# Performance work log

Hardware: AMD Instinct MI355X
Metric: run time of the kernel (lower is better)

The kernel has to match this reference:

```python
import math
import jax, jax.numpy as jnp
import numpy as np

B, N, D_MODEL, H = 2, 4096, 2048, 16
HEAD_DIM = D_MODEL // H
CHUNK = 128  # chunk length for the lightning-attention recurrence


def _slopes(n_heads):
    # ALiBi-style slopes used by lightning attention (n_heads is a power of 2)
    start = 2.0 ** (-(2.0 ** -(math.log2(n_heads) - 3)))
    return np.array([start ** (i + 1) for i in range(n_heads)], dtype=np.float32)


def setup_inputs() -> dict:
    key = jax.random.key(0)
    kx, k1, k2, k3, k4 = jax.random.split(key, 5)
    scale = 1.0 / math.sqrt(D_MODEL)
    x = jax.random.normal(kx, (B, N, D_MODEL), dtype=jnp.float32)
    w_qkv = jax.random.normal(k1, (3 * D_MODEL, D_MODEL), dtype=jnp.float32) * scale
    b_qkv = jax.random.normal(k2, (3 * D_MODEL,), dtype=jnp.float32) * 0.01
    w_out = jax.random.normal(k3, (D_MODEL, D_MODEL), dtype=jnp.float32) * scale
    b_out = jax.random.normal(k4, (D_MODEL,), dtype=jnp.float32) * 0.01
    return {"x": x, "w_qkv": w_qkv, "b_qkv": b_qkv, "w_out": w_out, "b_out": b_out}


def _lightning_attn(q, k, v):
    # q,k,v: (B, H, N, d). Causal linear attention with per-head decay lam:
    #   S_t = lam * S_{t-1} + k_t v_t^T ;  o_t = q_t S_t
    b, h, n, d = q.shape
    nc = n // CHUNK
    lam = jnp.exp(-jnp.asarray(_slopes(h)))  # (H,)

    pos = jnp.arange(CHUNK, dtype=jnp.float32)
    decay_q = lam[:, None] ** (pos + 1.0)            # (H, C) inter-chunk q scaling
    decay_k = lam[:, None] ** (CHUNK - 1.0 - pos)    # (H, C) state-update k scaling
    diff = pos[:, None] - pos[None, :]
    causal = diff >= 0
    dmask = jnp.where(causal, lam[:, None, None] ** jnp.maximum(diff, 0.0), 0.0)  # (H,C,C)
    lam_c = lam ** CHUNK                              # (H,)

    def to_chunks(t):
        return t.reshape(b, h, nc, CHUNK, d).transpose(2, 0, 1, 3, 4)  # (nc,B,H,C,d)

    qc, kc, vc = to_chunks(q), to_chunks(k), to_chunks(v)

    def step(S, inp):
        qb, kb, vb = inp  # each (B,H,C,d); S: (B,H,d,d)
        inter = jnp.einsum('bhcd,bhde->bhce', qb * decay_q[None, :, :, None], S)
        scores = jnp.einsum('bhcd,bhed->bhce', qb, kb) * dmask[None]
        intra = jnp.einsum('bhce,bhed->bhcd', scores, vb)
        S_new = lam_c[None, :, None, None] * S + jnp.einsum(
            'bhcd,bhce->bhde', kb * decay_k[None, :, :, None], vb)
        return S_new, inter + intra

    S0 = jnp.zeros((b, h, d, d), dtype=q.dtype)
    _, out = jax.lax.scan(step, S0, (qc, kc, vc))  # out: (nc,B,H,C,d)
    return out.transpose(1, 2, 0, 3, 4).reshape(b, h, n, d)


def reference(x, w_qkv, b_qkv, w_out, b_out):
    b, n, dm = x.shape
    qkv = x @ w_qkv.T + b_qkv                         # (B,N,3D)
    q, k, v = jnp.split(qkv, 3, axis=-1)
    def heads(t):
        return t.reshape(b, n, H, HEAD_DIM).transpose(0, 2, 1, 3)  # (B,H,N,d)
    attn = _lightning_attn(heads(q), heads(k), heads(v))
    attn = attn.transpose(0, 2, 1, 3).reshape(b, n, dm)
    return attn @ w_out.T + b_out
```

## Files before the change

### kernel.cpp

```cpp
#include <hip/hip_runtime.h>
#include <stdint.h>

#define DM    2048
#define NSEQ  4096
#define BB    2
#define NH    16
#define HD    128
#define CHK   128
#define NCHK  32
#define NBH   (BB*NH)
#define MTOT  (BB*NSEQ)
#define N3    (3*DM)

typedef unsigned short u16;
typedef unsigned int   u32;
typedef __attribute__((ext_vector_type(8))) short s16x8;
typedef __attribute__((ext_vector_type(4))) short s16x4;
typedef __attribute__((ext_vector_type(4))) float f32x4;
typedef __attribute__((ext_vector_type(2))) unsigned short u16x2;

__device__ __forceinline__ float b2f(u16 b){ u32 u = ((u32)b) << 16; float f; __builtin_memcpy(&f,&u,4); return f; }
__device__ __forceinline__ u16 f2b(float f){ u32 u; __builtin_memcpy(&u,&f,4); u += 0x7fffu + ((u>>16)&1u); return (u16)(u>>16); }

__device__ __forceinline__ void gload16(const u16* g, u16* l){
  __builtin_amdgcn_global_load_lds((const __attribute__((address_space(1))) void*)g,
                                   (__attribute__((address_space(3))) void*)l, 16, 0, 0);
}

__global__ __launch_bounds__(256) void conv_bf16(const float* __restrict__ src,
                                                 u16* __restrict__ dst, int n4)
{
  for (int i = blockIdx.x*blockDim.x + threadIdx.x; i < n4; i += gridDim.x*blockDim.x){
    f32x4 v = *(const f32x4*)(src + (size_t)i*4);
    s16x4 o;
    #pragma unroll
    for (int j=0;j<4;j++) o[j] = (short)f2b(v[j]);
    *(s16x4*)(dst + (size_t)i*4) = o;
  }
}


#define GEMM256_CORE(GA_, GB_)                                                  \
  const int tid  = threadIdx.x;                                                 \
  const int lane = tid & 63;                                                    \
  const int w    = tid >> 6;                                                    \
  const int wm_i = w >> 2, wn_i = w & 3;                                        \
  int bx = blockIdx.x, by = blockIdx.y;                                         \
  { const int gx = gridDim.x; const int nwg = gx*gridDim.y;                     \
    const int cpx = nwg >> 3; const int lin = by*gx + bx;                       \
    const int t_ = (lin & 7)*cpx + (lin >> 3);                                  \
    bx = t_ % gx; by = t_ / gx; }                                               \
  const int m0 = by << 8;                                                       \
  const int n0 = bx << 8;                                                       \
                  \
  const int q_  = (lane*16) ^ (((lane>>5)&1) << 5);                             \
  const int sgr = q_ >> 6;                                                      \
  const int sgc = (q_ & 63) >> 1;                                               \
  const u16* gA = GA_ + (size_t)(m0 + w*32 + sgr)*DM + sgc;                     \
  const u16* gB = GB_ + (size_t)(n0 + w*32 + sgr)*DM + sgc;                     \
  const int l15 = lane & 15, lg = lane >> 4;                                    \
  const int swz = ((lg*16) ^ (((l15>>3)&1) << 5)) >> 1;          \
  const int arow = (wm_i*128 + l15)*32 + swz;                                   \
  const int brow = (wn_i*64  + l15)*32 + swz;                                   \
  f32x4 acc[8][4];                                                              \
  _Pragma("unroll")                                                             \
  for (int m=0;m<8;m++)                                                         \
    _Pragma("unroll")                                                           \
    for (int n=0;n<4;n++) acc[m][n] = f32x4{0.f,0.f,0.f,0.f};                   \
  auto STAGE_A = [&](int set, int kt){                                          \
    const u16* a = gA + kt*32;                                                  \
    u16* la = lds + set + w*1024;                                               \
    gload16(a,         la);                                                     \
    gload16(a + 16*DM, la + 512);                                               \
  };                                                                            \
  auto STAGE_B = [&](int set, int kt){                                          \
    const u16* b = gB + kt*32;                                                  \
    u16* la = lds + set + w*1024;                                               \
    gload16(b,         la + 8192);                                              \
    gload16(b + 16*DM, la + 8704);                                              \
  };                                                                            \
  STAGE_A(0, 0);     STAGE_B(0, 0);                                             \
  STAGE_A(16384, 1); STAGE_B(16384, 1);                                         \
  STAGE_A(32768, 2); STAGE_B(32768, 2);                                         \
  asm volatile("s_waitcnt vmcnt(8)" ::: "memory");                              \
  __builtin_amdgcn_s_barrier();                                                 \
  int s0=0, s1=16384, s2=32768, s3=49152;                                       \
  for (int t=0; t<64; ++t){                                                     \
    const u16* base = lds + s0;                                                 \
         \
    s16x8 af0[4], af1[4], bfr[4];                                               \
    _Pragma("unroll")                                                           \
    for (int n=0;n<4;n++) bfr[n] = *(const s16x8*)(base + 8192 + brow + n*512); \
    _Pragma("unroll")                                                           \
    for (int m=0;m<4;m++) af0[m] = *(const s16x8*)(base + arow + m*512);        \
    if (t < 61) STAGE_A(s3, t+3);                                               \
    __builtin_amdgcn_sched_barrier(0);                                          \
    __builtin_amdgcn_s_barrier();                                               \
    asm volatile("s_waitcnt lgkmcnt(0)" ::: "memory");                          \
    __builtin_amdgcn_sched_barrier(0);                                          \
    __builtin_amdgcn_s_setprio(1);                                              \
    _Pragma("unroll")                                                           \
    for (int m=0;m<4;m++)                                                       \
      _Pragma("unroll")                                                         \
      for (int n=0;n<4;n++)                                                     \
        acc[m][n] = __builtin_amdgcn_mfma_f32_16x16x32_bf16(af0[m], bfr[n], acc[m][n], 0,0,0); \
    __builtin_amdgcn_s_setprio(0);                                              \
    __builtin_amdgcn_sched_barrier(0);                                          \
    __builtin_amdgcn_s_barrier();                                               \
      \
    _Pragma("unroll")                                                           \
    for (int m=0;m<4;m++) af1[m] = *(const s16x8*)(base + arow + (m+4)*512);    \
    if (t < 61) STAGE_B(s3, t+3);                                               \
    if      (t < 61)  { asm volatile("s_waitcnt vmcnt(8)" ::: "memory"); }      \
    else if (t == 61) { asm volatile("s_waitcnt vmcnt(4)" ::: "memory"); }      \
    else if (t == 62) { asm volatile("s_waitcnt vmcnt(0)" ::: "memory"); }      \
    __builtin_amdgcn_sched_barrier(0);                                          \
    __builtin_amdgcn_s_barrier();                                               \
    asm volatile("s_waitcnt lgkmcnt(0)" ::: "memory");                          \
    __builtin_amdgcn_sched_barrier(0);                                          \
    __builtin_amdgcn_s_setprio(1);                                              \
    _Pragma("unroll")                                                           \
    for (int m=0;m<4;m++)                                                       \
      _Pragma("unroll")                                                         \
      for (int n=0;n<4;n++)                                                     \
        acc[m+4][n] = __builtin_amdgcn_mfma_f32_16x16x32_bf16(af1[m], bfr[n], acc[m+4][n], 0,0,0); \
    __builtin_amdgcn_s_setprio(0);                                              \
    __builtin_amdgcn_sched_barrier(0);                                          \
    __builtin_amdgcn_s_barrier();                                               \
    const int tmp=s0; s0=s1; s1=s2; s2=s3; s3=tmp;                              \
  }

__global__ __launch_bounds__(512, 2) void gemm_qkv(const u16* __restrict__ Xb,
    const u16* __restrict__ Wb, const float* __restrict__ bias,
    u16* __restrict__ Qb, u16* __restrict__ Kb, u16* __restrict__ Vb)
{
  __shared__ u16 lds[4*16384];
  GEMM256_CORE(Xb, Wb)

  #pragma unroll
  for (int n=0;n<4;n++){
    const int gn = n0 + wn_i*64 + n*16 + l15;
    const float bv = bias[gn];
    const int which = gn >> 11;
    const int h = (gn >> 7) & 15;
    const int e = gn & 127;
    u16* base_ = (which==0) ? Qb : ((which==1) ? Kb : Vb);
    #pragma unroll
    for (int m=0;m<8;m++){
      #pragma unroll
      for (int r=0;r<4;r++){
        const int gm = m0 + wm_i*128 + m*16 + lg*4 + r;
        const int b  = gm >> 12;
        const int tt = gm & (NSEQ-1);
        base_[(((size_t)(b*NH + h))*NSEQ + tt)*HD + e] = f2b(acc[m][n][r] + bv);
      }
    }
  }
}

__global__ __launch_bounds__(512, 2) void gemm_out(const u16* __restrict__ Ab,
    const u16* __restrict__ Wb, const float* __restrict__ bias,
    float* __restrict__ Out)
{
  __shared__ u16 lds[4*16384];
  GEMM256_CORE(Ab, Wb)

  #pragma unroll
  for (int n=0;n<4;n++){
    const int gn = n0 + wn_i*64 + n*16 + l15;
    const float bv = bias[gn];
    #pragma unroll
    for (int m=0;m<8;m++){
      #pragma unroll
      for (int r=0;r<4;r++){
        const int gm = m0 + wm_i*128 + m*16 + lg*4 + r;
        Out[(size_t)gm*DM + gn] = acc[m][n][r] + bv;
      }
    }
  }
}

__global__ __launch_bounds__(256) void chunk_kv(const u16* __restrict__ Kb,
    const u16* __restrict__ Vb, u16* __restrict__ USb)
{
  __shared__ short Kt[128][152];
  __shared__ short Vt[128][152];
  const int tid = threadIdx.x;
  const int blk = blockIdx.x;
  const int c  = blk & (NCHK-1);
  const int bh = blk >> 5;
  const int h  = bh & (NH-1);
  const float slope = exp2f(-0.5f*(float)(h+1));

  const u16* kg = Kb + ((size_t)bh*NSEQ + (size_t)c*CHK)*HD;
  const u16* vg = Vb + ((size_t)bh*NSEQ + (size_t)c*CHK)*HD;

  const int e0 = (tid & 63) * 2;
  const int tq = tid >> 6;
  #pragma unroll
  for (int it=0; it<4; it++){
    const int tb = it*32 + tq*8;
    s16x8 k0v, k1v, v0v, v1v;
    #pragma unroll
    for (int j=0;j<8;j++){
      const int t = tb + j;
      u16x2 kv = *(const u16x2*)(kg + (size_t)t*HD + e0);
      u16x2 vv = *(const u16x2*)(vg + (size_t)t*HD + e0);
      const float dk = expf(-slope*(float)(CHK-1-t));
      k0v[j] = (short)f2b(b2f(kv[0])*dk);
      k1v[j] = (short)f2b(b2f(kv[1])*dk);
      v0v[j] = (short)vv[0];
      v1v[j] = (short)vv[1];
    }
    *(s16x8*)&Kt[e0  ][tb] = k0v;
    *(s16x8*)&Kt[e0+1][tb] = k1v;
    *(s16x8*)&Vt[e0  ][tb] = v0v;
    *(s16x8*)&Vt[e0+1][tb] = v1v;
  }
  __syncthreads();

  const int lane = tid & 63;
  const int l15 = lane & 15, lg = lane >> 4;
  const int w = tid >> 6;
  const int wm = (w >> 1) << 6, wn = (w & 1) << 6;
  f32x4 acc[4][4];
  #pragma unroll
  for (int i=0;i<4;i++)
    #pragma unroll
    for (int j=0;j<4;j++) acc[i][j] = f32x4{0.f,0.f,0.f,0.f};

  #pragma unroll
  for (int ks=0; ks<4; ks++){
    const int kk = ks*32 + lg*8;
    s16x8 af[4], bf[4];
    #pragma unroll
    for (int m=0;m<4;m++) af[m] = *(const s16x8*)&Kt[wm + m*16 + l15][kk];
    #pragma unroll
    for (int n=0;n<4;n++) bf[n] = *(const s16x8*)&Vt[wn + n*16 + l15][kk];
    #pragma unroll
    for (int m=0;m<4;m++)
      #pragma unroll
      for (int n=0;n<4;n++)
        acc[m][n] = __builtin_amdgcn_mfma_f32_16x16x32_bf16(af[m], bf[n], acc[m][n], 0,0,0);
  }

  u16* up = USb + (size_t)blk*(HD*HD);
  #pragma unroll
  for (int m=0;m<4;m++)
    #pragma unroll
    for (int n=0;n<4;n++)
      #pragma unroll
      for (int r=0;r<4;r++){
        const int d = wm + m*16 + lg*4 + r;
        const int f = wn + n*16 + l15;
        up[d*HD + f] = f2b(acc[m][n][r]);
      }
}

__global__ __launch_bounds__(256) void scan_state(u16* __restrict__ USb)
{
  const int bh = blockIdx.x >> 3;
  const int rs = blockIdx.x & 7;
  const int tid = threadIdx.x;
  const int h = bh & (NH-1);
  const float slope = exp2f(-0.5f*(float)(h+1));
  const float lamC = expf(-slope*(float)CHK);
  float s[8];
  #pragma unroll
  for (int i=0;i<8;i++) s[i]=0.f;
  u16* base = USb + (size_t)bh*NCHK*HD*HD + rs*2048;
  const int off = tid*8;
  for (int c=0;c<NCHK;c++){
    u16* p = base + (size_t)c*HD*HD + off;
    s16x8 u = *(const s16x8*)p;
    s16x8 wv;
    #pragma unroll
    for (int j=0;j<8;j++) wv[j] = (short)f2b(s[j]);
    *(s16x8*)p = wv;
    #pragma unroll
    for (int j=0;j<8;j++) s[j] = lamC*s[j] + b2f((u16)u[j]);
  }
}

__global__ __launch_bounds__(512) void attn_chunk(
    const u16* __restrict__ Qb, const u16* __restrict__ Kb, const u16* __restrict__ Vb,
    const u16* __restrict__ Sb, u16* __restrict__ ATT)
{
  __shared__ short lds[73728];
  short* Qs = lds;
  short* Ks = lds + 17408;
  short* Vt = lds + 34816;
  short* St = lds + 54272;

  const int tid = threadIdx.x;
  const int blk = blockIdx.x;
  const int c  = blk & (NCHK-1);
  const int bh = blk >> 5;
  const int b  = bh >> 4, h = bh & 15;
  const float slope = exp2f(-0.5f*(float)(h+1));

  const size_t qoff = ((size_t)bh*NSEQ + (size_t)c*CHK)*HD;

  #pragma unroll
  for (int i=0;i<4;i++){
    const int lin = i*4096 + tid*8;
    const int r = lin >> 7, e = lin & 127;
    *(s16x8*)&Qs[r*136 + e] = *(const s16x8*)(Qb + qoff + lin);
    *(s16x8*)&Ks[r*136 + e] = *(const s16x8*)(Kb + qoff + lin);
  }
  {
    const int f0 = (tid & 63)*2;
    const int tq = tid >> 6;
    const u16* vg = Vb + qoff;
    const u16* sg = Sb + ((size_t)bh*NCHK + c)*HD*HD;
    #pragma unroll
    for (int it=0; it<2; it++){
      const int t0 = it*64 + tq*8;
      s16x8 v0v, v1v, s0v, s1v;
      #pragma unroll
      for (int j=0;j<8;j++){
        u16x2 v2 = *(const u16x2*)(vg + (size_t)(t0+j)*HD + f0);
        u16x2 s2 = *(const u16x2*)(sg + (size_t)(t0+j)*HD + f0);
        v0v[j]=(short)v2[0]; v1v[j]=(short)v2[1];
        s0v[j]=(short)s2[0]; s1v[j]=(short)s2[1];
      }
      *(s16x8*)&Vt[(f0  )*152 + t0] = v0v;
      *(s16x8*)&Vt[(f0+1)*152 + t0] = v1v;
      *(s16x8*)&St[(f0  )*152 + t0] = s0v;
      *(s16x8*)&St[(f0+1)*152 + t0] = s1v;
    }
  }
  __syncthreads();

  const int lane = tid & 63;
  const int l15 = lane & 15, lg = lane >> 4;
  const int w = tid >> 6;
  const int wrow = (w >> 1) << 5;
  const int wcol = (w & 1) << 6;

  f32x4 accs[2][4], acco[2][4];
  #pragma unroll
  for (int m=0;m<2;m++)
    #pragma unroll
    for (int n=0;n<4;n++){ accs[m][n]=f32x4{0.f,0.f,0.f,0.f}; acco[m][n]=f32x4{0.f,0.f,0.f,0.f}; }

  #pragma unroll
  for (int ks=0; ks<4; ks++){
    const int kk = ks*32 + lg*8;
    s16x8 qa[2], kb_[4], sb_[4];
    #pragma unroll
    for (int m=0;m<2;m++) qa[m] = *(const s16x8*)&Qs[(wrow + m*16 + l15)*136 + kk];
    #pragma unroll
    for (int n=0;n<4;n++){
      kb_[n] = *(const s16x8*)&Ks[(wcol + n*16 + l15)*136 + kk];
      sb_[n] = *(const s16x8*)&St[(wcol + n*16 + l15)*152 + kk];
    }
    #pragma unroll
    for (int m=0;m<2;m++)
      #pragma unroll
      for (int n=0;n<4;n++){
        accs[m][n] = __builtin_amdgcn_mfma_f32_16x16x32_bf16(qa[m], kb_[n], accs[m][n], 0,0,0);
        acco[m][n] = __builtin_amdgcn_mfma_f32_16x16x32_bf16(qa[m], sb_[n], acco[m][n], 0,0,0);
      }
  }
  __syncthreads();

  #pragma unroll
  for (int m=0;m<2;m++){
    #pragma unroll
    for (int r=0;r<4;r++){
      const int t = wrow + m*16 + lg*4 + r;
      const float dq = expf(-slope*(float)(t+1));
      #pragma unroll
      for (int n=0;n<4;n++){
        const int s = wcol + n*16 + l15;
        float v = accs[m][n][r];
        v = (t >= s) ? v*expf(-slope*(float)(t-s)) : 0.f;
        Ks[t*136 + s] = (short)f2b(v);
        acco[m][n][r] *= dq;
      }
    }
  }
  __syncthreads();

  #pragma unroll
  for (int ks=0; ks<4; ks++){
    const int kk = ks*32 + lg*8;
    s16x8 sa[2], vb_[4];
    #pragma unroll
    for (int m=0;m<2;m++) sa[m] = *(const s16x8*)&Ks[(wrow + m*16 + l15)*136 + kk];
    #pragma unroll
    for (int n=0;n<4;n++) vb_[n] = *(const s16x8*)&Vt[(wcol + n*16 + l15)*152 + kk];
    #pragma unroll
    for (int m=0;m<2;m++)
      #pragma unroll
      for (int n=0;n<4;n++)
        acco[m][n] = __builtin_amdgcn_mfma_f32_16x16x32_bf16(sa[m], vb_[n], acco[m][n], 0,0,0);
  }

  u16* op = ATT + ((size_t)(b*NSEQ + c*CHK))*DM + h*HD;
  #pragma unroll
  for (int m=0;m<2;m++)
    #pragma unroll
    for (int n=0;n<4;n++)
      #pragma unroll
      for (int r=0;r<4;r++){
        const int t = wrow + m*16 + lg*4 + r;
        const int f = wcol + n*16 + l15;
        op[(size_t)t*DM + f] = f2b(acco[m][n][r]);
      }
}

extern "C" void kernel_launch(void* const* d_in, const int* in_sizes, int n_in,
                              void* d_out, int out_size, void* d_ws, size_t ws_size,
                              hipStream_t stream)
{
  const float* x     = (const float*)d_in[0];
  const float* w_qkv = (const float*)d_in[1];
  const float* b_qkv = (const float*)d_in[2];
  const float* w_out = (const float*)d_in[3];
  const float* b_out = (const float*)d_in[4];
  float* out = (float*)d_out;

  char* ws = (char*)d_ws;
  const size_t SZ = (size_t)MTOT * DM * sizeof(u16);
  u16* Qb    = (u16*)(ws);
  u16* Kb    = (u16*)(ws + SZ);
  u16* Vb    = (u16*)(ws + 2*SZ);
  u16* USb   = (u16*)(ws + 3*SZ);
  u16* ATT   = (u16*)(ws + 4*SZ);
  u16* Xb    = ATT;
  u16* Wqkvb = USb;
  u16* Woutb = Kb;

  conv_bf16 <<<dim3(2048), 256, 0, stream>>>(x,     Xb,    MTOT*DM/4);
  conv_bf16 <<<dim3(2048), 256, 0, stream>>>(w_qkv, Wqkvb, N3*DM/4);
  gemm_qkv  <<<dim3(N3/256,  MTOT/256), 512, 0, stream>>>(Xb, Wqkvb, b_qkv, Qb, Kb, Vb);
  chunk_kv  <<<dim3(NBH*NCHK),          256, 0, stream>>>(Kb, Vb, USb);
  scan_state<<<dim3(NBH*8),             256, 0, stream>>>(USb);
  attn_chunk<<<dim3(NBH*NCHK),          512, 0, stream>>>(Qb, Kb, Vb, USb, ATT);
  conv_bf16 <<<dim3(1024), 256, 0, stream>>>(w_out, Woutb, DM*DM/4);
  gemm_out  <<<dim3(DM/256,  MTOT/256), 512, 0, stream>>>(ATT, Woutb, b_out, out);
}
```

Before: 397.5 us.

## Stage QKV GEMM epilogue through LDS for coalesced stores; drop tile swizzle

The QKV GEMM epilogue used to write bf16 outputs one scalar at a time with a strided head-major layout. It now stages each 128-row half tile in shared memory and writes contiguous 16-byte vectors per row into the Q/K/V buffers. This is meant to cut the number of uncoalesced global writes. The block-index remap that grouped tiles for L2 locality is also removed from both GEMMs, which may hurt cache reuse. The extra barriers and LDS round trip add epilogue latency.

```diff
diff --git a/kernel.cpp b/kernel.cpp
--- a/kernel.cpp
+++ b/kernel.cpp
@@ -41,18 +41,13 @@
 
 
 #define GEMM256_CORE(GA_, GB_)                                                  \
+  __shared__ u16 lds[65536];                                       \
   const int tid  = threadIdx.x;                                                 \
   const int lane = tid & 63;                                                    \
   const int w    = tid >> 6;                                                    \
   const int wm_i = w >> 2, wn_i = w & 3;                                        \
-  int bx = blockIdx.x, by = blockIdx.y;                                         \
-  { const int gx = gridDim.x; const int nwg = gx*gridDim.y;                     \
-    const int cpx = nwg >> 3; const int lin = by*gx + bx;                       \
-    const int t_ = (lin & 7)*cpx + (lin >> 3);                                  \
-    bx = t_ % gx; by = t_ / gx; }                                               \
-  const int m0 = by << 8;                                                       \
-  const int n0 = bx << 8;                                                       \
-                  \
+  const int m0 = blockIdx.y << 8;                                               \
+  const int n0 = blockIdx.x << 8;                                               \
   const int q_  = (lane*16) ^ (((lane>>5)&1) << 5);                             \
   const int sgr = q_ >> 6;                                                      \
   const int sgc = (q_ & 63) >> 1;                                               \
@@ -87,10 +82,10 @@
   int s0=0, s1=16384, s2=32768, s3=49152;                                       \
   for (int t=0; t<64; ++t){                                                     \
     const u16* base = lds + s0;                                                 \
-         \
-    s16x8 af0[4], af1[4], bfr[4];                                               \
-    _Pragma("unroll")                                                           \
-    for (int n=0;n<4;n++) bfr[n] = *(const s16x8*)(base + 8192 + brow + n*512); \
+    s16x8 bf[4], af0[4], af1[4];                                                \
+            \
+    _Pragma("unroll")                                                           \
+    for (int n=0;n<4;n++) bf[n]  = *(const s16x8*)(base + 8192 + brow + n*512); \
     _Pragma("unroll")                                                           \
     for (int m=0;m<4;m++) af0[m] = *(const s16x8*)(base + arow + m*512);        \
     if (t < 61) STAGE_A(s3, t+3);                                               \
@@ -103,7 +98,7 @@
     for (int m=0;m<4;m++)                                                       \
       _Pragma("unroll")                                                         \
       for (int n=0;n<4;n++)                                                     \
-        acc[m][n] = __builtin_amdgcn_mfma_f32_16x16x32_bf16(af0[m], bfr[n], acc[m][n], 0,0,0); \
+        acc[m][n] = __builtin_amdgcn_mfma_f32_16x16x32_bf16(af0[m], bf[n], acc[m][n], 0,0,0); \
     __builtin_amdgcn_s_setprio(0);                                              \
     __builtin_amdgcn_sched_barrier(0);                                          \
     __builtin_amdgcn_s_barrier();                                               \
@@ -123,7 +118,7 @@
     for (int m=0;m<4;m++)                                                       \
       _Pragma("unroll")                                                         \
       for (int n=0;n<4;n++)                                                     \
-        acc[m+4][n] = __builtin_amdgcn_mfma_f32_16x16x32_bf16(af1[m], bfr[n], acc[m+4][n], 0,0,0); \
+        acc[m+4][n] = __builtin_amdgcn_mfma_f32_16x16x32_bf16(af1[m], bf[n], acc[m+4][n], 0,0,0); \
     __builtin_amdgcn_s_setprio(0);                                              \
     __builtin_amdgcn_sched_barrier(0);                                          \
     __builtin_amdgcn_s_barrier();                                               \
@@ -134,27 +129,42 @@
     const u16* __restrict__ Wb, const float* __restrict__ bias,
     u16* __restrict__ Qb, u16* __restrict__ Kb, u16* __restrict__ Vb)
 {
-  __shared__ u16 lds[4*16384];
   GEMM256_CORE(Xb, Wb)
 
-  #pragma unroll
-  for (int n=0;n<4;n++){
-    const int gn = n0 + wn_i*64 + n*16 + l15;
-    const float bv = bias[gn];
-    const int which = gn >> 11;
-    const int h = (gn >> 7) & 15;
-    const int e = gn & 127;
-    u16* base_ = (which==0) ? Qb : ((which==1) ? Kb : Vb);
-    #pragma unroll
-    for (int m=0;m<8;m++){
-      #pragma unroll
-      for (int r=0;r<4;r++){
-        const int gm = m0 + wm_i*128 + m*16 + lg*4 + r;
-        const int b  = gm >> 12;
-        const int tt = gm & (NSEQ-1);
-        base_[(((size_t)(b*NH + h))*NSEQ + tt)*HD + e] = f2b(acc[m][n][r] + bv);
-      }
-    }
+  __syncthreads();
+  float bv[4];
+  #pragma unroll
+  for (int n=0;n<4;n++) bv[n] = bias[n0 + wn_i*64 + n*16 + l15];
+
+  #pragma unroll
+  for (int p=0;p<2;p++){
+    if (wm_i == p){
+      #pragma unroll
+      for (int m=0;m<8;m++)
+        #pragma unroll
+        for (int n=0;n<4;n++)
+          #pragma unroll
+          for (int r=0;r<4;r++)
+            lds[(m*16 + lg*4 + r)*264 + wn_i*64 + n*16 + l15] = f2b(acc[m][n][r] + bv[n]);
+    }
+    __syncthreads();
+    {
+      const int r2 = tid >> 2;
+      const int c4 = (tid & 3) * 64;
+      const int gm = m0 + p*128 + r2;
+      const int b  = gm >> 12;
+      const int tt = gm & (NSEQ-1);
+      const int gn0 = n0 + c4;
+      const int which = gn0 >> 11;
+      const int h  = (gn0 >> 7) & 15;
+      const int e0 = gn0 & 127;
+      u16* bp = ((which==0)?Qb:((which==1)?Kb:Vb))
+                + (((size_t)(b*NH + h))*NSEQ + tt)*HD + e0;
+      #pragma unroll
+      for (int j=0;j<8;j++)
+        *(s16x8*)(bp + j*8) = *(const s16x8*)(lds + r2*264 + c4 + j*8);
+    }
+    __syncthreads();
   }
 }
 
@@ -162,7 +172,6 @@
     const u16* __restrict__ Wb, const float* __restrict__ bias,
     float* __restrict__ Out)
 {
-  __shared__ u16 lds[4*16384];
   GEMM256_CORE(Ab, Wb)
 
   #pragma unroll
@@ -286,11 +295,11 @@
     const u16* __restrict__ Qb, const u16* __restrict__ Kb, const u16* __restrict__ Vb,
     const u16* __restrict__ Sb, u16* __restrict__ ATT)
 {
-  __shared__ short lds[73728];
-  short* Qs = lds;
-  short* Ks = lds + 17408;
-  short* Vt = lds + 34816;
-  short* St = lds + 54272;
+  __shared__ short alds[73728];
+  short* Qs = alds;
+  short* Ks = alds + 17408;
+  short* Vt = alds + 34816;
+  short* St = alds + 54272;
 
   const int tid = threadIdx.x;
   const int blk = blockIdx.x;
```

New measurement: 407.3 us. +2.5%, slower.
